# Kernel optimization log

Measured on AMD Instinct MI355X. Metric: run time of the kernel, lower is better.

The kernel has to match this reference:

```python
import jax, jax.numpy as jnp
import numpy as np

NHEAD = 16
NEG1 = -9e15   # first masked_fill value (-9000000000000000.0)
NEG2 = -9e16   # second masked_fill value


def setup_inputs() -> dict:
    key = jax.random.key(0)
    ks = jax.random.split(key, 8)
    slen, bsz, emb = 512, 16, 1024
    x = jax.random.normal(ks[0], (slen, bsz, emb), dtype=jnp.float32)
    mask = jax.random.randint(ks[1], (bsz, slen, slen), 0, 2, dtype=jnp.int32)
    weight_mask = jax.random.randint(ks[2], (bsz, slen, slen), 0, 2, dtype=jnp.int32)
    s = 1.0 / np.sqrt(emb)
    Wq = jax.random.normal(ks[3], (emb, emb), dtype=jnp.float32) * s
    Wk = jax.random.normal(ks[4], (emb, emb), dtype=jnp.float32) * s
    Wv = jax.random.normal(ks[5], (emb, emb), dtype=jnp.float32) * s
    Ws = jax.random.normal(ks[6], (emb, emb), dtype=jnp.float32) * s
    Wb = jax.random.normal(ks[7], (1, 3 * emb), dtype=jnp.float32) * s
    return {"x": x, "mask": mask, "weight_mask": weight_mask,
            "Wq": Wq, "Wk": Wk, "Wv": Wv, "Ws": Ws, "Wb": Wb}


def reference(x, mask, weight_mask, Wq, Wk, Wv, Ws, Wb):
    slen, bsz, emb = x.shape
    hd = emb // NHEAD
    scaling = float(hd) ** -0.5

    def split_heads(t):  # (slen, bsz, emb) -> (bsz, nhead, slen, hd)
        return t.reshape(slen, bsz, NHEAD, hd).transpose(1, 2, 0, 3)

    q = split_heads(x @ Wq.T)
    k = split_heads(x @ Wk.T)
    v = split_heads(x @ Wv.T)

    attn = jnp.einsum('bhqd,bhkd->bhqk', q, k) * scaling

    m = mask.astype(attn.dtype)[:, None, :, :]          # (bsz,1,slen,slen)
    attn = jnp.where(m == 0, NEG1, attn)
    attn = jax.nn.softmax(attn, axis=-1) * m

    wm = weight_mask.astype(attn.dtype)[:, None, :, :]
    attn = jnp.where(wm == 0, NEG2, attn)
    attn = jax.nn.softmax(attn, axis=-1) * wm
    # degree normalization: row-normalize
    attn = attn * (1.0 / (attn.sum(-1) + 1e-10))[..., None]

    # dropout inactive (eval mode)
    out = jnp.einsum('bhqk,bhkd->bhqd', attn, v)         # (bsz,nhead,slen,hd)
    out = out.transpose(2, 0, 1, 3).reshape(slen, bsz, emb)

    r = x @ Ws.T
    gate = jax.nn.sigmoid(jnp.concatenate([out, r, out - r], axis=-1) @ Wb.T)
    return gate * r + (1.0 - gate) * out
```

## Files before the change

kernel.cpp:

```cpp
#include <hip/hip_runtime.h>
#include <hip/hip_bf16.h>
#include <stdint.h>

typedef __attribute__((ext_vector_type(8))) short short8;
typedef __attribute__((ext_vector_type(4))) float f32x4;
typedef __attribute__((ext_vector_type(4))) unsigned short ushort4v;

#define MFMA_BF16(a,b,c) __builtin_amdgcn_mfma_f32_16x16x32_bf16((a),(b),(c),0,0,0)

static __device__ __forceinline__ unsigned short f2bf(float f){
  union { float fv; unsigned int u; } c; c.fv = f;
  unsigned int u = c.u;
  return (unsigned short)((u + 0x7fffu + ((u >> 16) & 1u)) >> 16);
}

static __device__ __forceinline__ unsigned int cvtpk(float a, float b){
  unsigned int r;
  asm("v_cvt_pk_bf16_f32 %0, %1, %2" : "=v"(r) : "v"(a), "v"(b));
  return r;
}

static __device__ __forceinline__ void gload_lds16(const void* g, void* l){
  __builtin_amdgcn_global_load_lds(
      (const __attribute__((address_space(1))) void*)g,
      (__attribute__((address_space(3))) void*)l, 16, 0, 0);
}

static __device__ __forceinline__ float wred_sum(float v){
  #pragma unroll
  for (int m = 32; m; m >>= 1) v += __shfl_xor(v, m, 64);
  return v;
}

static __device__ __forceinline__ void unpack8(uint4 u, float* f){
  f[0] = __uint_as_float(u.x << 16); f[1] = __uint_as_float(u.x & 0xFFFF0000u);
  f[2] = __uint_as_float(u.y << 16); f[3] = __uint_as_float(u.y & 0xFFFF0000u);
  f[4] = __uint_as_float(u.z << 16); f[5] = __uint_as_float(u.z & 0xFFFF0000u);
  f[6] = __uint_as_float(u.w << 16); f[7] = __uint_as_float(u.w & 0xFFFF0000u);
}

__global__ __launch_bounds__(256) void cvt_x_kernel(const float* __restrict__ x,
                                                    unsigned short* __restrict__ o){
  int i = blockIdx.x * 256 + threadIdx.x;
  float4 f = ((const float4*)x)[i];
  ushort4v r;
  r[0] = f2bf(f.x); r[1] = f2bf(f.y); r[2] = f2bf(f.z); r[3] = f2bf(f.w);
  ((ushort4v*)o)[i] = r;
}

__global__ __launch_bounds__(256) void cvt_w_kernel(const float* __restrict__ Wq,
                                                    const float* __restrict__ Wk,
                                                    const float* __restrict__ Wv,
                                                    const float* __restrict__ Ws,
                                                    unsigned short* __restrict__ B){
  int i = blockIdx.x * 256 + threadIdx.x;
  int which = i >> 18;
  const float* src = (which == 0) ? Wq : (which == 1) ? Wk : (which == 2) ? Wv : Ws;
  float4 f = ((const float4*)src)[i & 262143];
  ushort4v r;
  r[0] = f2bf(f.x); r[1] = f2bf(f.y); r[2] = f2bf(f.z); r[3] = f2bf(f.w);
  ((ushort4v*)B)[i] = r;
}

__global__ void wb_prep_kernel(const float* __restrict__ Wb,
                               float* __restrict__ wba, float* __restrict__ wbb){
  int e = blockIdx.x * 256 + threadIdx.x;
  if (e < 1024){
    wba[e] = Wb[e]        + Wb[2048 + e];
    wbb[e] = Wb[1024 + e] - Wb[2048 + e];
  }
}

__global__ __launch_bounds__(256) void mask_prep_kernel(
    const int* __restrict__ m, const int* __restrict__ wm,
    unsigned long long* __restrict__ mb, unsigned long long* __restrict__ wb)
{
  const size_t i = (size_t)blockIdx.x * 256 + threadIdx.x;
  const int a = m[i];
  const int c = wm[i];
  unsigned long long ba = __ballot(a != 0);
  unsigned long long bc = __ballot(c != 0);
  if ((threadIdx.x & 63) == 0){
    mb[i >> 6] = ba;
    wb[i >> 6] = bc;
  }
}

__global__ __launch_bounds__(512, 1) void gemm_proj_kernel(
    const unsigned short* __restrict__ X, const unsigned short* __restrict__ B,
    unsigned short* __restrict__ qb, unsigned short* __restrict__ kb,
    unsigned short* __restrict__ vT, unsigned short* __restrict__ rbb)
{
  __shared__ __align__(16) unsigned short smem[73728];
  const int tid = threadIdx.x;
  const int w = tid >> 6, l = tid & 63;
  const int lr = l & 15, lq = l >> 4;
  const int wm = w >> 1, wn = w & 1;
  const int xcd = blockIdx.x & 7, o = blockIdx.x >> 3;
  const int mt = xcd * 4 + (o & 3), nt = o >> 2;
  const int m0 = mt * 256, n0 = nt * 128;
  const int lrow8 = l >> 3, lc = l & 7;

  f32x4 acc[4][4] = {};

  #define STAGE_H(T, H) { \
    const int bufo_ = ((T) % 3) * 24576; \
    const int kk_ = (T) * 64; \
    _Pragma("unroll") \
    for (int j = (H) * 2; j < (H) * 2 + 2; j++){ \
      const int seg = w + j * 8; \
      const int r = seg * 8 + lrow8; \
      gload_lds16(X + (size_t)(m0 + r) * 1024 + kk_ + ((lc ^ (r & 7)) * 8), \
                  smem + bufo_ + seg * 512); \
    } \
    { \
      const int seg = w + (H) * 8; \
      const int r = seg * 8 + lrow8; \
      gload_lds16(B + (size_t)(n0 + r) * 1024 + kk_ + ((lc ^ (r & 7)) * 8), \
                  smem + bufo_ + 16384 + seg * 512); \
    } }

  #define PHASE(T, SUBK, DOSTAGE) { \
    const int bo_ = ((T) % 3) * 24576; \
    short8 av[4], bv[4]; \
    const int pc = ((((SUBK) * 4 + lq) ^ (lr & 7)) * 8); \
    _Pragma("unroll") \
    for (int mf = 0; mf < 4; mf++) \
      av[mf] = *(const short8*)(smem + bo_ + (wm * 64 + mf * 16 + lr) * 64 + pc); \
    _Pragma("unroll") \
    for (int nf = 0; nf < 4; nf++) \
      bv[nf] = *(const short8*)(smem + bo_ + 16384 + (wn * 64 + nf * 16 + lr) * 64 + pc); \
    if (DOSTAGE) STAGE_H((T) + 2, SUBK) \
    asm volatile("s_waitcnt lgkmcnt(0)" ::: "memory"); \
    __builtin_amdgcn_sched_barrier(0); \
    __builtin_amdgcn_s_setprio(1); \
    _Pragma("unroll") \
    for (int mf = 0; mf < 4; mf++) \
      _Pragma("unroll") \
      for (int nf = 0; nf < 4; nf++) \
        acc[mf][nf] = MFMA_BF16(av[mf], bv[nf], acc[mf][nf]); \
    __builtin_amdgcn_s_setprio(0); }

  STAGE_H(0, 0) STAGE_H(0, 1)
  STAGE_H(1, 0) STAGE_H(1, 1)

  for (int t = 0; t < 15; t++){
    asm volatile("s_waitcnt vmcnt(6)" ::: "memory");
    __builtin_amdgcn_s_barrier();
    const bool st = (t < 14);
    PHASE(t, 0, st)
    __builtin_amdgcn_s_barrier();
    PHASE(t, 1, st)
  }
  asm volatile("s_waitcnt vmcnt(0)" ::: "memory");
  __builtin_amdgcn_s_barrier();
  PHASE(15, 0, false)
  PHASE(15, 1, false)

  const int which = nt >> 3;
  const int o0 = (nt & 7) * 128;
  if (which == 2){
    __syncthreads();
    #pragma unroll
    for (int mf = 0; mf < 4; mf++)
      #pragma unroll
      for (int nf = 0; nf < 4; nf++){
        const int c = wn * 64 + nf * 16 + lr;
        const int r0v = wm * 64 + mf * 16 + lq * 4;
        uint2 pk;
        pk.x = cvtpk(acc[mf][nf][0], acc[mf][nf][1]);
        pk.y = cvtpk(acc[mf][nf][2], acc[mf][nf][3]);
        *(uint2*)(smem + c * 264 + r0v) = pk;
      }
    __syncthreads();
    #pragma unroll
    for (int p = 0; p < 8; p++){
      const int cid = p * 512 + tid;
      const int c = cid >> 5, bb = (cid >> 1) & 15, sh = cid & 1;
      short8 st;
      #pragma unroll
      for (int j = 0; j < 8; j++) st[j] = (short)smem[c * 264 + (sh * 8 + j) * 16 + bb];
      const int oo = o0 + c;
      const int bh = bb * 16 + (oo >> 6), d = oo & 63;
      *(short8*)(vT + ((size_t)bh * 64 + d) * 512 + mt * 16 + sh * 8) = st;
    }
  } else {
    #pragma unroll
    for (int h2 = 0; h2 < 2; h2++){
      __syncthreads();
      if ((wm >> 1) == h2){
        #pragma unroll
        for (int mf = 0; mf < 4; mf++)
          #pragma unroll
          for (int nf = 0; nf < 4; nf++)
            #pragma unroll
            for (int rg = 0; rg < 4; rg++)
              smem[((wm & 1) * 64 + mf * 16 + lq * 4 + rg) * 136 + wn * 64 + nf * 16 + lr]
                  = f2bf(acc[mf][nf][rg]);
      }
      __syncthreads();
      if (which == 3){
        #pragma unroll
        for (int p = 0; p < 4; p++){
          const int cid = p * 512 + tid;
          const int lrow = cid >> 4, cg = cid & 15;
          short8 vv = *(const short8*)(smem + lrow * 136 + cg * 8);
          *(short8*)(rbb + (size_t)(m0 + h2 * 128 + lrow) * 1024 + o0 + cg * 8) = vv;
        }
      } else {
        unsigned short* dst = (which == 0) ? qb : kb;
        #pragma unroll
        for (int p = 0; p < 4; p++){
          const int cid = p * 512 + tid;
          const int lrow = cid >> 4, cg = cid & 15;
          short8 vv = *(const short8*)(smem + lrow * 136 + cg * 8);
          const int rowi = m0 + h2 * 128 + lrow;
          const int s = rowi >> 4, bb = rowi & 15;
          const int oo = o0 + cg * 8;
          const int bh = bb * 16 + (oo >> 6), d = oo & 63;
          *(short8*)(dst + ((size_t)bh * 512 + s) * 64 + d) = vv;
        }
      }
    }
  }
  #undef STAGE_H
  #undef PHASE
}

__global__ __launch_bounds__(256, 4) void attn_kernel(
    const unsigned short* __restrict__ qg, const unsigned short* __restrict__ kg,
    const unsigned short* __restrict__ vt,
    const unsigned char* __restrict__ mbits, const unsigned char* __restrict__ wbits,
    unsigned short* __restrict__ outp)
{
  __shared__ __align__(16) unsigned short sE[32 * 520];
  __shared__ float sfin[32];
  const int bid = ((blockIdx.x & 7) << 9) | (blockIdx.x >> 3);
  const int qt = bid & 15, h = (bid >> 4) & 15, b = bid >> 8;
  const int tid = threadIdx.x, w = tid >> 6, l = tid & 63;
  const int lr = l & 15, lq = l >> 4;
  const int bh = b * 16 + h;
  const unsigned short* qp = qg + ((size_t)bh * 512 + qt * 32) * 64;
  const unsigned short* kp = kg + (size_t)bh * 512 * 64;
  const unsigned short* vp = vt + (size_t)bh * 64 * 512;

  const unsigned char* mrb = mbits + ((size_t)(b * 512 + qt * 32)) * 64;
  const unsigned char* wrb = wbits + ((size_t)(b * 512 + qt * 32)) * 64;
  unsigned int mby[2][4], wby[2][4];
  #pragma unroll
  for (int g = 0; g < 2; g++)
    #pragma unroll
    for (int rr = 0; rr < 4; rr++){
      mby[g][rr] = mrb[(g * 16 + w * 4 + rr) * 64 + l];
      wby[g][rr] = wrb[(g * 16 + w * 4 + rr) * 64 + l];
    }

  short8 qa[2][2];
  #pragma unroll
  for (int t = 0; t < 2; t++){
    qa[t][0] = *(const short8*)(qp + (t * 16 + lr) * 64 + lq * 8);
    qa[t][1] = *(const short8*)(qp + (t * 16 + lr) * 64 + 32 + lq * 8);
  }
  const float CEXP = 0.18033688011112042f;
  #pragma unroll
  for (int kf = 0; kf < 8; kf++){
    const unsigned short* kr = kp + (size_t)(w * 128 + kf * 16 + lr) * 64;
    short8 k0 = *(const short8*)(kr + lq * 8);
    short8 k1 = *(const short8*)(kr + 32 + lq * 8);
    f32x4 a0 = {}, a1 = {};
    a0 = MFMA_BF16(qa[0][0], k0, a0);
    a1 = MFMA_BF16(qa[1][0], k0, a1);
    a0 = MFMA_BF16(qa[0][1], k1, a0);
    a1 = MFMA_BF16(qa[1][1], k1, a1);
    const int col = w * 128 + kf * 16 + lr;
    #pragma unroll
    for (int t = 0; t < 2; t++){
      f32x4 a = t ? a1 : a0;
      float e0 = __builtin_amdgcn_exp2f(a[0] * CEXP);
      float e1 = __builtin_amdgcn_exp2f(a[1] * CEXP);
      float e2 = __builtin_amdgcn_exp2f(a[2] * CEXP);
      float e3 = __builtin_amdgcn_exp2f(a[3] * CEXP);
      unsigned int p01 = cvtpk(e0, e1), p23 = cvtpk(e2, e3);
      const int row = t * 16 + lq * 4;
      sE[(row    ) * 520 + col] = (unsigned short)(p01 & 0xFFFFu);
      sE[(row + 1) * 520 + col] = (unsigned short)(p01 >> 16);
      sE[(row + 2) * 520 + col] = (unsigned short)(p23 & 0xFFFFu);
      sE[(row + 3) * 520 + col] = (unsigned short)(p23 >> 16);
    }
  }
  __syncthreads();

  #pragma unroll
  for (int g = 0; g < 2; g++){
    const int row0 = g * 16 + w * 4;
    uint4 ev[4];
    #pragma unroll
    for (int rr = 0; rr < 4; rr++)
      ev[rr] = *(const uint4*)(sE + (row0 + rr) * 520 + l * 8);

    float em[4][8]; float z1[4];
    #pragma unroll
    for (int rr = 0; rr < 4; rr++){
      float e1[8];
      unpack8(ev[rr], e1);
      const unsigned int mb = mby[g][rr];
      float z = 0.f;
      #pragma unroll
      for (int j = 0; j < 8; j++){
        em[rr][j] = ((mb >> j) & 1u) ? e1[j] : 0.f;
        z += em[rr][j];
      }
      z1[rr] = z;
    }
    #pragma unroll
    for (int m = 32; m; m >>= 1){
      #pragma unroll
      for (int rr = 0; rr < 4; rr++) z1[rr] += __shfl_xor(z1[rr], m, 64);
    }
    float e2[4][8]; float z2[4];
    #pragma unroll
    for (int rr = 0; rr < 4; rr++){
      const float i1L = 1.4426950408889634f / z1[rr];
      const unsigned int wv = wby[g][rr];
      float z = 0.f;
      #pragma unroll
      for (int j = 0; j < 8; j++){
        float t = __builtin_amdgcn_exp2f(em[rr][j] * i1L);
        e2[rr][j] = ((wv >> j) & 1u) ? t : 0.f;
        z += e2[rr][j];
      }
      z2[rr] = z;
    }
    #pragma unroll
    for (int m = 32; m; m >>= 1){
      #pragma unroll
      for (int rr = 0; rr < 4; rr++) z2[rr] += __shfl_xor(z2[rr], m, 64);
    }
    #pragma unroll
    for (int rr = 0; rr < 4; rr++){
      uint4 oo;
      oo.x = cvtpk(e2[rr][0], e2[rr][1]); oo.y = cvtpk(e2[rr][2], e2[rr][3]);
      oo.z = cvtpk(e2[rr][4], e2[rr][5]); oo.w = cvtpk(e2[rr][6], e2[rr][7]);
      *(uint4*)(sE + (row0 + rr) * 520 + l * 8) = oo;
      if (l == 0) sfin[row0 + rr] = 1.f / (z2[rr] + 1e-10f);
    }
  }
  __syncthreads();

  {
    f32x4 po0 = {}, po1 = {};
    #pragma unroll
    for (int ks = 0; ks < 16; ks++){
      short8 vf = *(const short8*)(vp + (size_t)(w * 16 + lr) * 512 + ks * 32 + lq * 8);
      short8 af0 = *(const short8*)(sE + (     lr) * 520 + ks * 32 + lq * 8);
      short8 af1 = *(const short8*)(sE + (16 + lr) * 520 + ks * 32 + lq * 8);
      po0 = MFMA_BF16(af0, vf, po0);
      po1 = MFMA_BF16(af1, vf, po1);
    }
    #pragma unroll
    for (int rg = 0; rg < 4; rg++){
      const int r0 = lq * 4 + rg;
      outp[((size_t)(qt * 32 + r0) * 16 + b) * 1024 + h * 64 + w * 16 + lr]
          = f2bf(po0[rg] * sfin[r0]);
      outp[((size_t)(qt * 32 + 16 + r0) * 16 + b) * 1024 + h * 64 + w * 16 + lr]
          = f2bf(po1[rg] * sfin[16 + r0]);
    }
  }
}

__global__ __launch_bounds__(256) void gate_kernel(
    const unsigned short* __restrict__ outp, const unsigned short* __restrict__ rbb,
    const float* __restrict__ wba, const float* __restrict__ wbb,
    float* __restrict__ y)
{
  const int t = blockIdx.x * 4 + (threadIdx.x >> 6);
  const int l = threadIdx.x & 63;
  const unsigned short* o = outp + (size_t)t * 1024;
  const unsigned short* r = rbb + (size_t)t * 1024;
  float ov[16], rv[16];
  float acc = 0.f;
  #pragma unroll
  for (int j = 0; j < 16; j++){
    const int e = j * 64 + l;
    ov[j] = __uint_as_float((unsigned int)o[e] << 16);
    rv[j] = __uint_as_float((unsigned int)r[e] << 16);
    acc += ov[j] * wba[e] + rv[j] * wbb[e];
  }
  const float dot = wred_sum(acc);
  const float g = 1.f / (1.f + __builtin_amdgcn_exp2f(-dot * 1.4426950408889634f));
  float* yo = y + (size_t)t * 1024;
  #pragma unroll
  for (int j = 0; j < 16; j++){
    const int e = j * 64 + l;
    yo[e] = g * rv[j] + (1.f - g) * ov[j];
  }
}

extern "C" void kernel_launch(void* const* d_in, const int* in_sizes, int n_in,
                              void* d_out, int out_size, void* d_ws, size_t ws_size,
                              hipStream_t stream)
{
  (void)in_sizes; (void)n_in; (void)out_size; (void)ws_size;
  const float* x   = (const float*)d_in[0];
  const int* mask  = (const int*)d_in[1];
  const int* wmask = (const int*)d_in[2];
  const float* Wq  = (const float*)d_in[3];
  const float* Wk  = (const float*)d_in[4];
  const float* Wv  = (const float*)d_in[5];
  const float* Ws  = (const float*)d_in[6];
  const float* Wb  = (const float*)d_in[7];

  char* ws = (char*)d_ws;
  unsigned short* xbf = (unsigned short*)ws; ws += 16777216;
  unsigned short* bm  = (unsigned short*)ws; ws += 8388608;
  unsigned short* qb  = (unsigned short*)ws; ws += 16777216;
  unsigned short* kb  = (unsigned short*)ws; ws += 16777216;
  unsigned short* vT  = (unsigned short*)ws; ws += 16777216;
  unsigned short* rbb = (unsigned short*)ws; ws += 16777216;
  unsigned short* op  = (unsigned short*)ws; ws += 16777216;
  float* wba = (float*)ws; ws += 4096;
  float* wbb = (float*)ws; ws += 4096;
  unsigned long long* mb64 = (unsigned long long*)xbf;
  unsigned long long* wb64 = (unsigned long long*)bm;

  cvt_x_kernel<<<8192, 256, 0, stream>>>(x, xbf);
  cvt_w_kernel<<<4096, 256, 0, stream>>>(Wq, Wk, Wv, Ws, bm);
  wb_prep_kernel<<<4, 256, 0, stream>>>(Wb, wba, wbb);
  gemm_proj_kernel<<<1024, 512, 0, stream>>>(xbf, bm, qb, kb, vT, rbb);
  mask_prep_kernel<<<16384, 256, 0, stream>>>(mask, wmask, mb64, wb64);
  attn_kernel<<<4096, 256, 0, stream>>>(qb, kb, vT,
      (const unsigned char*)mb64, (const unsigned char*)wb64, op);
  gate_kernel<<<2048, 256, 0, stream>>>(op, rbb, wba, wbb, (float*)d_out);
}
```

Baseline: 177.8 us.

## Keep attention scores in registers across both masked softmaxes

Each wave now applies the first mask, exponentiates, and sums row partials straight from its MFMA accumulator registers. The second masked softmax also runs in registers, and the mask bits are loaded as 64-bit words aligned to each lane's column layout. Only the final weights are written to LDS, and cross-wave row sums go through two small LDS buffers. This removes a round trip of the intermediate exponentials through LDS and their bf16 rounding. In exchange it holds many more registers, so the launch-bounds occupancy hint drops from 4 to 3 blocks per CU.

```diff
diff --git a/kernel.cpp b/kernel.cpp
--- a/kernel.cpp
+++ b/kernel.cpp
@@ -30,13 +30,6 @@
   #pragma unroll
   for (int m = 32; m; m >>= 1) v += __shfl_xor(v, m, 64);
   return v;
-}
-
-static __device__ __forceinline__ void unpack8(uint4 u, float* f){
-  f[0] = __uint_as_float(u.x << 16); f[1] = __uint_as_float(u.x & 0xFFFF0000u);
-  f[2] = __uint_as_float(u.y << 16); f[3] = __uint_as_float(u.y & 0xFFFF0000u);
-  f[4] = __uint_as_float(u.z << 16); f[5] = __uint_as_float(u.z & 0xFFFF0000u);
-  f[6] = __uint_as_float(u.w << 16); f[7] = __uint_as_float(u.w & 0xFFFF0000u);
 }
 
 __global__ __launch_bounds__(256) void cvt_x_kernel(const float* __restrict__ x,
@@ -227,14 +220,15 @@
   #undef PHASE
 }
 
-__global__ __launch_bounds__(256, 4) void attn_kernel(
+__global__ __launch_bounds__(256, 3) void attn_kernel(
     const unsigned short* __restrict__ qg, const unsigned short* __restrict__ kg,
     const unsigned short* __restrict__ vt,
     const unsigned char* __restrict__ mbits, const unsigned char* __restrict__ wbits,
     unsigned short* __restrict__ outp)
 {
   __shared__ __align__(16) unsigned short sE[32 * 520];
-  __shared__ float sfin[32];
+  __shared__ float zbuf1[128];
+  __shared__ float zbuf2[128];
   const int bid = ((blockIdx.x & 7) << 9) | (blockIdx.x >> 3);
   const int qt = bid & 15, h = (bid >> 4) & 15, b = bid >> 8;
   const int tid = threadIdx.x, w = tid >> 6, l = tid & 63;
@@ -244,16 +238,17 @@
   const unsigned short* kp = kg + (size_t)bh * 512 * 64;
   const unsigned short* vp = vt + (size_t)bh * 64 * 512;
 
-  const unsigned char* mrb = mbits + ((size_t)(b * 512 + qt * 32)) * 64;
-  const unsigned char* wrb = wbits + ((size_t)(b * 512 + qt * 32)) * 64;
-  unsigned int mby[2][4], wby[2][4];
-  #pragma unroll
-  for (int g = 0; g < 2; g++)
-    #pragma unroll
-    for (int rr = 0; rr < 4; rr++){
-      mby[g][rr] = mrb[(g * 16 + w * 4 + rr) * 64 + l];
-      wby[g][rr] = wrb[(g * 16 + w * 4 + rr) * 64 + l];
-    }
+  const unsigned char* mbase = mbits + ((size_t)(b * 512 + qt * 32)) * 64;
+  const unsigned char* wbase = wbits + ((size_t)(b * 512 + qt * 32)) * 64;
+  unsigned long long mus[2][2][4];
+  #pragma unroll
+  for (int c = 0; c < 2; c++)
+    #pragma unroll
+    for (int t = 0; t < 2; t++)
+      #pragma unroll
+      for (int rg = 0; rg < 4; rg++)
+        mus[c][t][rg] = (*(const unsigned long long*)(mbase
+            + (size_t)(t * 16 + lq * 4 + rg) * 64 + (c * 4 + w) * 8)) >> lr;
 
   short8 qa[2][2];
   #pragma unroll
@@ -262,90 +257,122 @@
     qa[t][1] = *(const short8*)(qp + (t * 16 + lr) * 64 + 32 + lq * 8);
   }
   const float CEXP = 0.18033688011112042f;
-  #pragma unroll
-  for (int kf = 0; kf < 8; kf++){
-    const unsigned short* kr = kp + (size_t)(w * 128 + kf * 16 + lr) * 64;
-    short8 k0 = *(const short8*)(kr + lq * 8);
-    short8 k1 = *(const short8*)(kr + 32 + lq * 8);
-    f32x4 a0 = {}, a1 = {};
-    a0 = MFMA_BF16(qa[0][0], k0, a0);
-    a1 = MFMA_BF16(qa[1][0], k0, a1);
-    a0 = MFMA_BF16(qa[0][1], k1, a0);
-    a1 = MFMA_BF16(qa[1][1], k1, a1);
-    const int col = w * 128 + kf * 16 + lr;
-    #pragma unroll
-    for (int t = 0; t < 2; t++){
-      f32x4 a = t ? a1 : a0;
-      float e0 = __builtin_amdgcn_exp2f(a[0] * CEXP);
-      float e1 = __builtin_amdgcn_exp2f(a[1] * CEXP);
-      float e2 = __builtin_amdgcn_exp2f(a[2] * CEXP);
-      float e3 = __builtin_amdgcn_exp2f(a[3] * CEXP);
-      unsigned int p01 = cvtpk(e0, e1), p23 = cvtpk(e2, e3);
-      const int row = t * 16 + lq * 4;
-      sE[(row    ) * 520 + col] = (unsigned short)(p01 & 0xFFFFu);
-      sE[(row + 1) * 520 + col] = (unsigned short)(p01 >> 16);
-      sE[(row + 2) * 520 + col] = (unsigned short)(p23 & 0xFFFFu);
-      sE[(row + 3) * 520 + col] = (unsigned short)(p23 >> 16);
-    }
-  }
+  f32x4 em[2][2][4];
+  f32x4 z1p[2] = {};
+  #pragma unroll
+  for (int c = 0; c < 2; c++){
+    #pragma unroll
+    for (int kf = 0; kf < 4; kf++){
+      const unsigned short* kr = kp + (size_t)(c * 256 + w * 64 + kf * 16 + lr) * 64;
+      short8 k0 = *(const short8*)(kr + lq * 8);
+      short8 k1 = *(const short8*)(kr + 32 + lq * 8);
+      f32x4 a0 = {}, a1 = {};
+      a0 = MFMA_BF16(qa[0][0], k0, a0);
+      a1 = MFMA_BF16(qa[1][0], k0, a1);
+      a0 = MFMA_BF16(qa[0][1], k1, a0);
+      a1 = MFMA_BF16(qa[1][1], k1, a1);
+      #pragma unroll
+      for (int t = 0; t < 2; t++){
+        f32x4 a = t ? a1 : a0;
+        #pragma unroll
+        for (int rg = 0; rg < 4; rg++){
+          float e = __builtin_amdgcn_exp2f(a[rg] * CEXP);
+          const unsigned int bit = (unsigned int)(mus[c][t][rg] >> (kf * 16)) & 1u;
+          float v = bit ? e : 0.f;
+          em[c][t][kf][rg] = v;
+          z1p[t][rg] += v;
+        }
+      }
+    }
+  }
+  #pragma unroll
+  for (int mm = 1; mm <= 8; mm <<= 1)
+    #pragma unroll
+    for (int t = 0; t < 2; t++)
+      #pragma unroll
+      for (int rg = 0; rg < 4; rg++)
+        z1p[t][rg] += __shfl_xor(z1p[t][rg], mm, 64);
+  if (lr == 0){
+    #pragma unroll
+    for (int t = 0; t < 2; t++)
+      #pragma unroll
+      for (int rg = 0; rg < 4; rg++)
+        zbuf1[(t * 16 + lq * 4 + rg) * 4 + w] = z1p[t][rg];
+  }
+  unsigned long long wus[2][2][4];
+  #pragma unroll
+  for (int c = 0; c < 2; c++)
+    #pragma unroll
+    for (int t = 0; t < 2; t++)
+      #pragma unroll
+      for (int rg = 0; rg < 4; rg++)
+        wus[c][t][rg] = (*(const unsigned long long*)(wbase
+            + (size_t)(t * 16 + lq * 4 + rg) * 64 + (c * 4 + w) * 8)) >> lr;
   __syncthreads();
 
-  #pragma unroll
-  for (int g = 0; g < 2; g++){
-    const int row0 = g * 16 + w * 4;
-    uint4 ev[4];
-    #pragma unroll
-    for (int rr = 0; rr < 4; rr++)
-      ev[rr] = *(const uint4*)(sE + (row0 + rr) * 520 + l * 8);
-
-    float em[4][8]; float z1[4];
-    #pragma unroll
-    for (int rr = 0; rr < 4; rr++){
-      float e1[8];
-      unpack8(ev[rr], e1);
-      const unsigned int mb = mby[g][rr];
-      float z = 0.f;
-      #pragma unroll
-      for (int j = 0; j < 8; j++){
-        em[rr][j] = ((mb >> j) & 1u) ? e1[j] : 0.f;
-        z += em[rr][j];
+  f32x4 il[2];
+  #pragma unroll
+  for (int t = 0; t < 2; t++)
+    #pragma unroll
+    for (int rg = 0; rg < 4; rg++){
+      float4 zz = *(const float4*)&zbuf1[(t * 16 + lq * 4 + rg) * 4];
+      il[t][rg] = 1.4426950408889634f / (zz.x + zz.y + zz.z + zz.w);
+    }
+
+  f32x4 z2p[2] = {};
+  #pragma unroll
+  for (int c = 0; c < 2; c++)
+    #pragma unroll
+    for (int kf = 0; kf < 4; kf++)
+      #pragma unroll
+      for (int t = 0; t < 2; t++)
+        #pragma unroll
+        for (int rg = 0; rg < 4; rg++){
+          float v = __builtin_amdgcn_exp2f(em[c][t][kf][rg] * il[t][rg]);
+          const unsigned int bit = (unsigned int)(wus[c][t][rg] >> (kf * 16)) & 1u;
+          float v2 = bit ? v : 0.f;
+          em[c][t][kf][rg] = v2;
+          z2p[t][rg] += v2;
+        }
+  #pragma unroll
+  for (int mm = 1; mm <= 8; mm <<= 1)
+    #pragma unroll
+    for (int t = 0; t < 2; t++)
+      #pragma unroll
+      for (int rg = 0; rg < 4; rg++)
+        z2p[t][rg] += __shfl_xor(z2p[t][rg], mm, 64);
+  if (lr == 0){
+    #pragma unroll
+    for (int t = 0; t < 2; t++)
+      #pragma unroll
+      for (int rg = 0; rg < 4; rg++)
+        zbuf2[(t * 16 + lq * 4 + rg) * 4 + w] = z2p[t][rg];
+  }
+  #pragma unroll
+  for (int c = 0; c < 2; c++)
+    #pragma unroll
+    for (int kf = 0; kf < 4; kf++)
+      #pragma unroll
+      for (int t = 0; t < 2; t++){
+        unsigned int p01 = cvtpk(em[c][t][kf][0], em[c][t][kf][1]);
+        unsigned int p23 = cvtpk(em[c][t][kf][2], em[c][t][kf][3]);
+        const int row = t * 16 + lq * 4;
+        const int col = c * 256 + w * 64 + kf * 16 + lr;
+        sE[(row    ) * 520 + col] = (unsigned short)(p01 & 0xFFFFu);
+        sE[(row + 1) * 520 + col] = (unsigned short)(p01 >> 16);
+        sE[(row + 2) * 520 + col] = (unsigned short)(p23 & 0xFFFFu);
+        sE[(row + 3) * 520 + col] = (unsigned short)(p23 >> 16);
       }
-      z1[rr] = z;
-    }
-    #pragma unroll
-    for (int m = 32; m; m >>= 1){
-      #pragma unroll
-      for (int rr = 0; rr < 4; rr++) z1[rr] += __shfl_xor(z1[rr], m, 64);
-    }
-    float e2[4][8]; float z2[4];
-    #pragma unroll
-    for (int rr = 0; rr < 4; rr++){
-      const float i1L = 1.4426950408889634f / z1[rr];
-      const unsigned int wv = wby[g][rr];
-      float z = 0.f;
-      #pragma unroll
-      for (int j = 0; j < 8; j++){
-        float t = __builtin_amdgcn_exp2f(em[rr][j] * i1L);
-        e2[rr][j] = ((wv >> j) & 1u) ? t : 0.f;
-        z += e2[rr][j];
-      }
-      z2[rr] = z;
-    }
-    #pragma unroll
-    for (int m = 32; m; m >>= 1){
-      #pragma unroll
-      for (int rr = 0; rr < 4; rr++) z2[rr] += __shfl_xor(z2[rr], m, 64);
-    }
-    #pragma unroll
-    for (int rr = 0; rr < 4; rr++){
-      uint4 oo;
-      oo.x = cvtpk(e2[rr][0], e2[rr][1]); oo.y = cvtpk(e2[rr][2], e2[rr][3]);
-      oo.z = cvtpk(e2[rr][4], e2[rr][5]); oo.w = cvtpk(e2[rr][6], e2[rr][7]);
-      *(uint4*)(sE + (row0 + rr) * 520 + l * 8) = oo;
-      if (l == 0) sfin[row0 + rr] = 1.f / (z2[rr] + 1e-10f);
-    }
-  }
   __syncthreads();
+
+  f32x4 fin[2];
+  #pragma unroll
+  for (int t = 0; t < 2; t++)
+    #pragma unroll
+    for (int rg = 0; rg < 4; rg++){
+      float4 zz = *(const float4*)&zbuf2[(t * 16 + lq * 4 + rg) * 4];
+      fin[t][rg] = 1.f / (zz.x + zz.y + zz.z + zz.w + 1e-10f);
+    }
 
   {
     f32x4 po0 = {}, po1 = {};
@@ -361,9 +388,9 @@
     for (int rg = 0; rg < 4; rg++){
       const int r0 = lq * 4 + rg;
       outp[((size_t)(qt * 32 + r0) * 16 + b) * 1024 + h * 64 + w * 16 + lr]
-          = f2bf(po0[rg] * sfin[r0]);
+          = f2bf(po0[rg] * fin[0][rg]);
       outp[((size_t)(qt * 32 + 16 + r0) * 16 + b) * 1024 + h * 64 + w * 16 + lr]
-          = f2bf(po1[rg] * sfin[16 + r0]);
+          = f2bf(po1[rg] * fin[1][rg]);
     }
   }
 }
```

New measurement: 193.5 us. 1.09x slower.
